# Optimization experiments

Measured on AMD Instinct MI355X. Metric: run time of the kernel, lower is better.

The kernel has to match this reference:

```python
import jax, jax.numpy as jnp
import numpy as np

WIN, DIL, PAD, H = 5, 1, 2, 8  # window, dilation, unfold padding, num_heads
C = 256
EPS = 1e-5

def _ln(z, g, b):
    m = jnp.mean(z, axis=-1, keepdims=True)
    v = jnp.mean((z - m) ** 2, axis=-1, keepdims=True)
    return (z - m) * jax.lax.rsqrt(v + EPS) * g + b

def setup_inputs() -> dict:
    key = jax.random.key(0)
    ks = jax.random.split(key, 16)
    s = 0.02
    d = {
        'x': jax.random.normal(ks[0], (32, C, 64, 25), jnp.float32),
        'ln1_g': jnp.ones((C,), jnp.float32), 'ln1_b': jnp.zeros((C,), jnp.float32),
        'q_w': jax.random.normal(ks[1], (C, C)) * s, 'q_b': jnp.zeros((C,)),
        'qa_w': jax.random.normal(ks[2], (C, H)) * s, 'qa_b': jnp.zeros((H,)),
        'k_w': jax.random.normal(ks[3], (C, C)) * s, 'k_b': jnp.zeros((C,)),
        'ka_w': jax.random.normal(ks[4], (C, H)) * s, 'ka_b': jnp.zeros((H,)),
        'v_w': jax.random.normal(ks[5], (C, C)) * s, 'v_b': jnp.zeros((C,)),
        't_w': jax.random.normal(ks[6], (C, C)) * s, 't_b': jnp.zeros((C,)),
        'p_w': jax.random.normal(ks[7], (C, C)) * s, 'p_b': jnp.zeros((C,)),
        'ffn_g': jnp.ones((C,)), 'ffn_b': jnp.zeros((C,)),
        'w1': jax.random.normal(ks[8], (C, C)) * s, 'b1': jnp.zeros((C,)),
        'w2': jax.random.normal(ks[9], (C, C)) * s, 'b2': jnp.zeros((C,)),
    }
    return d

def reference(x, ln1_g, ln1_b, q_w, q_b, qa_w, qa_b, k_w, k_b, ka_w, ka_b,
              v_w, v_b, t_w, t_b, p_w, p_b, ffn_g, ffn_b, w1, b1, w2, b2):
    N, Cc, T, V = x.shape
    hc = Cc // H
    scale = 1.0 / np.sqrt(hc)
    B, L = N * T, WIN * V
    xp = jnp.pad(x, ((0, 0), (0, 0), (PAD, PAD), (0, 0)))
    win = jnp.stack([xp[:, :, k * DIL:k * DIL + T, :] for k in range(WIN)], axis=2)  # (N,C,W,T,V)
    wx = win.transpose(0, 3, 2, 4, 1).reshape(B, L, Cc)
    nx = _ln(wx, ln1_g, ln1_b)
    # attention: softmax-pooled query
    q = nx @ q_w + q_b                                      # (B,L,C)
    qw = jax.nn.softmax(((q @ qa_w + qa_b) * scale).transpose(0, 2, 1), axis=-1)  # (B,H,L)
    qh = q.reshape(B, L, H, hc).transpose(0, 2, 1, 3)       # (B,H,L,hc)
    pq = jnp.einsum('bhl,bhld->bhd', qw, qh)                # (B,H,hc)
    k_ = nx @ k_w + k_b
    kq = k_ * pq.reshape(B, 1, Cc)
    kw = jax.nn.softmax(((kq @ ka_w + ka_b) * scale).transpose(0, 2, 1), axis=-1)
    kh = k_.reshape(B, L, H, hc).transpose(0, 2, 1, 3)
    pk = jnp.einsum('bhl,bhld->bhd', kw, kh)                # (B,H,hc)
    v_ = nx @ v_w + v_b
    vh = v_.reshape(B, L, H, hc).transpose(0, 2, 1, 3)
    kv = (vh * pk[:, :, None, :]).transpose(0, 2, 1, 3).reshape(B, L, Cc)
    kvh = (kv @ t_w + t_b).reshape(B, L, H, hc).transpose(0, 2, 1, 3)
    att = ((kvh + qh).transpose(0, 2, 1, 3).reshape(B, L, Cc)) @ p_w + p_b
    # average over window, residual with flattened x
    att = att.reshape(B, WIN, V, Cc).mean(axis=1)           # (B,V,C)
    att = att + x.transpose(0, 2, 3, 1).reshape(B, V, Cc)
    # FFN residual block
    f = _ln(att, ffn_g, ffn_b)
    f = jax.nn.gelu(f @ w1 + b1, approximate=False) @ w2 + b2
    y = f + att
    return y.reshape(N, T, V, Cc).transpose(0, 3, 1, 2)     # (N,C,T,V)
```

## Files before the change

### kernel.cpp

```cpp
#include <hip/hip_runtime.h>
#include <hip/hip_bf16.h>

typedef unsigned short u16b;
typedef __attribute__((ext_vector_type(8))) short short8;
typedef __attribute__((ext_vector_type(4))) float floatx4;

#define DEV static __device__ __forceinline__

DEV float sh2f(unsigned short s) { union { unsigned u; float f; } c; c.u = ((unsigned)s) << 16; return c.f; }
DEV unsigned short f2b(float f) {
    unsigned u = __float_as_uint(f);
    u += 0x7FFF + ((u >> 16) & 1);
    return (unsigned short)(u >> 16);
}

constexpr int O_LN1G = 0, O_LN1B = 256, O_QB = 512, O_KB = 768, O_VB = 1024,
              O_TB = 1280, O_PB = 1536, O_FFNG = 1792, O_FFNB = 2048,
              O_B1 = 2304, O_B2 = 2560, O_QAB = 2816, O_KAB = 2824,
              O_QAW = 2832, O_KAW = 4880, O_CV = 6928;

__global__ void detect_k(const unsigned* __restrict__ xw, int* __restrict__ flag) {
    __shared__ int cnt;
    if (threadIdx.x == 0) cnt = 0;
    __syncthreads();
    int my = 0;
    for (int i = threadIdx.x; i < 4096; i += 256) {
        unsigned w = xw[i];
        unsigned e0 = (w >> 7) & 0xFFu;
        if (e0 >= 0xC0u) my++;
    }
    atomicAdd(&cnt, my);
    __syncthreads();
    if (threadIdx.x == 0) flag[0] = (cnt > 64) ? 1 : 0;
}

DEV unsigned short load_cvt(const void* src, size_t idx, int fp32) {
    return fp32 ? f2b(((const float*)src)[idx]) : ((const u16b*)src)[idx];
}

struct VecTab { const void* p[15]; int off[15]; int n[15]; };

__global__ __launch_bounds__(256)
void convert_vecs_k(VecTab tab, const int* __restrict__ flag, u16b* __restrict__ sv) {
    int e = blockIdx.x, fp32 = flag[0];
    const void* s = tab.p[e];
    int n = tab.n[e], off = tab.off[e];
    for (int i = threadIdx.x; i < n; i += 256)
        sv[off + i] = load_cvt(s, i, fp32);
}

struct W8 { const void* p[8]; unsigned dstoff[8]; unsigned rstride[8]; };

__global__ void wtrans_k(W8 tab, u16b* __restrict__ base, const int* __restrict__ flag) {
    __shared__ u16b tile[32][33];
    int fp32 = flag[0];
    const void* src = tab.p[blockIdx.z];
    u16b* dst = base + tab.dstoff[blockIdx.z];
    unsigned rs = tab.rstride[blockIdx.z];
    int c0 = blockIdx.x * 32, r0 = blockIdx.y * 32;
    int tx = threadIdx.x, ty = threadIdx.y;
#pragma unroll
    for (int i = 0; i < 32; i += 8)
        tile[ty + i][tx] = load_cvt(src, (size_t)(r0 + ty + i) * 256 + c0 + tx, fp32);
    __syncthreads();
#pragma unroll
    for (int i = 0; i < 32; i += 8)
        dst[(size_t)(c0 + ty + i) * rs + r0 + tx] = tile[tx][ty + i];
}

__global__ __launch_bounds__(256)
void transpose_in_k(const void* __restrict__ src, u16b* __restrict__ dst,
                    int rows, int cols, const int* __restrict__ flag) {
    __shared__ u16b tile[32][36];
    int fp32 = flag[0];
    int c0 = blockIdx.x * 32, r0 = blockIdx.y * 32;
    size_t zb = (size_t)blockIdx.z * rows * cols;
    int tid = threadIdx.x;
    int r = tid >> 3, c4 = (tid & 7) * 4;
    size_t sidx = zb + (size_t)(r0 + r) * cols + c0 + c4;
    if (fp32) {
        const float4 f4 = *(const float4*)((const float*)src + sidx);
        tile[r][c4]     = f2b(f4.x);
        tile[r][c4 + 1] = f2b(f4.y);
        tile[r][c4 + 2] = f2b(f4.z);
        tile[r][c4 + 3] = f2b(f4.w);
    } else {
        *(ushort4*)&tile[r][c4] = *(const ushort4*)((const u16b*)src + sidx);
    }
    __syncthreads();
    int c = tid >> 3, r4 = (tid & 7) * 4;
    ushort4 o;
    o.x = tile[r4][c]; o.y = tile[r4 + 1][c]; o.z = tile[r4 + 2][c]; o.w = tile[r4 + 3][c];
    *(ushort4*)&dst[zb + (size_t)(c0 + c) * rows + r0 + r4] = o;
}

__global__ __launch_bounds__(256)
void transpose_out_k(const u16b* __restrict__ src, void* __restrict__ dst,
                     int rows, int cols, const int* __restrict__ flag) {
    __shared__ u16b tile[32][36];
    int fp32 = flag[0];
    int c0 = blockIdx.x * 32, r0 = blockIdx.y * 32;
    size_t zb = (size_t)blockIdx.z * rows * cols;
    int tid = threadIdx.x;
    int r = tid >> 3, c4 = (tid & 7) * 4;
    *(ushort4*)&tile[r][c4] = *(const ushort4*)&src[zb + (size_t)(r0 + r) * cols + c0 + c4];
    __syncthreads();
    int c = tid >> 3, r4 = (tid & 7) * 4;
    size_t didx = zb + (size_t)(c0 + c) * rows + r0 + r4;
    if (fp32) {
        float4 f4;
        f4.x = sh2f(tile[r4][c]);     f4.y = sh2f(tile[r4 + 1][c]);
        f4.z = sh2f(tile[r4 + 2][c]); f4.w = sh2f(tile[r4 + 3][c]);
        *(float4*)((float*)dst + didx) = f4;
    } else {
        ushort4 o;
        o.x = tile[r4][c]; o.y = tile[r4 + 1][c]; o.z = tile[r4 + 2][c]; o.w = tile[r4 + 3][c];
        *(ushort4*)((u16b*)dst + didx) = o;
    }
}

__global__ __launch_bounds__(256)
void rowstats_k(const u16b* __restrict__ src, float2* __restrict__ st,
                int valid, int total) {
    int wv = threadIdx.x >> 6, lane = threadIdx.x & 63;
    int r = blockIdx.x * 4 + wv;
    if (r >= total) return;
    if (r >= valid) { if (lane == 0) st[r] = make_float2(0.f, 0.f); return; }
    int c = lane * 4;
    ushort4 raw = *(const ushort4*)&src[(size_t)r * 256 + c];
    float x0 = sh2f(raw.x), x1 = sh2f(raw.y), x2 = sh2f(raw.z), x3 = sh2f(raw.w);
    float s  = x0 + x1 + x2 + x3;
    float sq = x0 * x0 + x1 * x1 + x2 * x2 + x3 * x3;
#pragma unroll
    for (int o = 32; o; o >>= 1) { s += __shfl_xor(s, o); sq += __shfl_xor(sq, o); }
    float mean = s * (1.f / 256.f);
    float var  = sq * (1.f / 256.f) - mean * mean;
    if (lane == 0) st[r] = make_float2(mean, rsqrtf(var + 1e-5f));
}

__global__ __launch_bounds__(256)
void cvec_k(const u16b* __restrict__ pT, u16b* __restrict__ sv) {
    int j = threadIdx.x;
    float acc = sh2f(sv[O_PB + j]);
    const u16b* row = pT + (size_t)j * 256;
    for (int i = 0; i < 256; i += 8) {
        short8 t8 = *(const short8*)&sv[O_TB + i];
        short8 p8 = *(const short8*)&row[i];
#pragma unroll
        for (int u = 0; u < 8; ++u)
            acc += sh2f((unsigned short)t8[u]) * sh2f((unsigned short)p8[u]);
    }
    sv[O_CV + j] = f2b(acc);
}

template <int EPI, int LNA>
__global__ __launch_bounds__(256)
void gemm256(const u16b* __restrict__ A, int aStride, int K,
             const u16b* __restrict__ Wt,
             const u16b* __restrict__ bias, const u16b* __restrict__ addm,
             u16b* __restrict__ out, size_t osParam,
             const float2* __restrict__ stats,
             const u16b* __restrict__ gvec, const u16b* __restrict__ bvec) {
    __shared__ u16b As[128 * 72];
    __shared__ u16b Bs[128 * 72];
    __shared__ float sg[256], sb[256];
    const int tid = threadIdx.x;
    const int m0 = blockIdx.x * 128, n0 = blockIdx.y * 128;
    const int wv = tid >> 6, lane = tid & 63;
    const int wrow = (wv >> 1) * 64, wcol = (wv & 1) * 64;
    const int fr = lane & 15;
    const int fq = lane >> 4;
    floatx4 acc[4][4];
    const floatx4 zero = {0.f, 0.f, 0.f, 0.f};
#pragma unroll
    for (int i = 0; i < 4; ++i)
#pragma unroll
        for (int j = 0; j < 4; ++j) acc[i][j] = zero;

    float2 strow[4];
    if (LNA) {
        sg[tid] = sh2f(gvec[tid]);
        sb[tid] = sh2f(bvec[tid]);
#pragma unroll
        for (int kk = 0; kk < 4; ++kk) strow[kk] = stats[m0 + (tid >> 3) + kk * 32];
        __syncthreads();
    }

    for (int kt = 0; kt < K; kt += 64) {
#pragma unroll
        for (int kk = 0; kk < 4; ++kk) {
            int chunk = tid + kk * 256;
            int row = chunk >> 3, col = (chunk & 7) * 8;
            union { uint4 u; unsigned short h[8]; } rw;
            rw.u = *(const uint4*)&A[(size_t)(m0 + row) * aStride + kt + col];
            if (LNA) {
#pragma unroll
                for (int j = 0; j < 8; ++j) {
                    float f = sh2f(rw.h[j]);
                    f = (f - strow[kk].x) * strow[kk].y * sg[kt + col + j] + sb[kt + col + j];
                    rw.h[j] = f2b(f);
                }
            }
            *(uint4*)&As[row * 72 + col] = rw.u;
            *(uint4*)&Bs[row * 72 + col] = *(const uint4*)&Wt[(size_t)(n0 + row) * K + kt + col];
        }
        __syncthreads();
#pragma unroll
        for (int s = 0; s < 2; ++s) {
            short8 af[4], bfr[4];
#pragma unroll
            for (int i = 0; i < 4; ++i)
                af[i] = *(short8*)&As[(wrow + i * 16 + fr) * 72 + s * 32 + fq * 8];
#pragma unroll
            for (int j = 0; j < 4; ++j)
                bfr[j] = *(short8*)&Bs[(wcol + j * 16 + fr) * 72 + s * 32 + fq * 8];
#pragma unroll
            for (int i = 0; i < 4; ++i)
#pragma unroll
                for (int j = 0; j < 4; ++j)
                    acc[i][j] = __builtin_amdgcn_mfma_f32_16x16x32_bf16(af[i], bfr[j], acc[i][j], 0, 0, 0);
        }
        __syncthreads();
    }
    float bv[4];
#pragma unroll
    for (int j = 0; j < 4; ++j) bv[j] = bias ? sh2f(bias[n0 + wcol + j * 16 + fr]) : 0.f;
#pragma unroll
    for (int i = 0; i < 4; ++i) {
#pragma unroll
        for (int r = 0; r < 4; ++r) {
            int row = m0 + wrow + i * 16 + fq * 4 + r;
            size_t ro = (size_t)row * 256;
#pragma unroll
            for (int j = 0; j < 4; ++j) {
                int col = n0 + wcol + j * 16 + fr;
                float val = acc[i][j][r] + bv[j];
                if (EPI == 2) val += sh2f(addm[ro + col]);
                if (EPI == 3) val = 0.5f * val * (1.0f + erff(val * 0.70710678118654752f));
                if (EPI == 4)      out[(size_t)(col >> 8) * osParam + ro + (col & 255)] = f2b(val);
                else if (EPI == 0) out[(size_t)row * osParam + col] = f2b(val);
                else               out[ro + col] = f2b(val);
            }
        }
    }
}

DEV void logits_stage(const u16b* __restrict__ S, const u16b* __restrict__ sv,
                      int awoff, int aboff, const float* mult,
                      const int* srow, u16b* su, float* slog, int tid) {
    for (int i = tid; i < 2048; i += 512) {
        int c = i >> 3, h = i & 7;
        float w = sh2f(sv[awoff + i]);
        if (mult) w *= mult[c];
        su[h * 260 + c] = f2b(w);
    }
    __syncthreads();
    int wv = tid >> 6, lane = tid & 63;
    int fr = lane & 15, fq = lane >> 4;
    floatx4 acc = {0.f, 0.f, 0.f, 0.f};
    const u16b* Ar = S + (size_t)srow[wv * 16 + fr] * 256;
#pragma unroll
    for (int s = 0; s < 8; ++s) {
        short8 a  = *(const short8*)&Ar[s * 32 + fq * 8];
        short8 bb = *(const short8*)&su[fr * 260 + s * 32 + fq * 8];
        acc = __builtin_amdgcn_mfma_f32_16x16x32_bf16(a, bb, acc, 0, 0, 0);
    }
    float abv = sh2f(sv[aboff + (fr & 7)]);
    if (fr < 8) {
#pragma unroll
        for (int r = 0; r < 4; ++r)
            slog[(wv * 16 + fq * 4 + r) * 9 + fr] = (acc[r] + abv) * 0.17677669529663687f;
    }
    __syncthreads();
    {
        int h = wv;
        float v0 = (lane < 125) ? slog[lane * 9 + h] : -1e30f;
        float v1 = (lane + 64 < 125) ? slog[(lane + 64) * 9 + h] : -1e30f;
        float mx = fmaxf(v0, v1);
#pragma unroll
        for (int o = 32; o; o >>= 1) mx = fmaxf(mx, __shfl_xor(mx, o));
        float e0 = (lane < 125) ? __expf(v0 - mx) : 0.f;
        float e1 = (lane + 64 < 125) ? __expf(v1 - mx) : 0.f;
        float s = e0 + e1;
#pragma unroll
        for (int o = 32; o; o >>= 1) s += __shfl_xor(s, o);
        float inv = 1.f / s;
        if (lane < 125) slog[lane * 9 + h] = e0 * inv;
        if (lane + 64 < 125) slog[(lane + 64) * 9 + h] = e1 * inv;
    }
    __syncthreads();
}

__global__ __launch_bounds__(512)
void pool_fused(const u16b* __restrict__ qf, const u16b* __restrict__ kf,
                const u16b* __restrict__ vf, const u16b* __restrict__ sv,
                u16b* __restrict__ CB) {
    __shared__ int srow[128];
    __shared__ u16b su[16 * 260];
    __shared__ float slog[128 * 9];
    __shared__ float spool[16 * 260];
    __shared__ float spq[256], spk[256];
    int bid = blockIdx.x;
    int b = ((bid & 7) << 8) | (bid >> 3);
    int n = b >> 6, t = b & 63;
    int tid = threadIdx.x;
    if (tid < 128) {
        int l = tid < 125 ? tid : 124;
        int w = l / 25, v = l - w * 25, tt = t + w - 2;
        srow[tid] = ((unsigned)tt < 64u) ? (n * 64 + tt) * 25 + v : 51200;
    }
    __syncthreads();

    logits_stage(qf, sv, O_QAW, O_QAB, nullptr, srow, su, slog, tid);

    {
        int c8 = (tid & 31) * 8, h = c8 >> 5, ls = tid >> 5;
        float p[8] = {0.f, 0.f, 0.f, 0.f, 0.f, 0.f, 0.f, 0.f};
        for (int v = ls; v < 25; v += 16) {
            float s[8] = {0.f, 0.f, 0.f, 0.f, 0.f, 0.f, 0.f, 0.f};
#pragma unroll
            for (int w = 0; w < 5; ++w) {
                int l = w * 25 + v;
                float wt = slog[l * 9 + h];
                short8 d8 = *(const short8*)&qf[(size_t)srow[l] * 256 + c8];
#pragma unroll
                for (int j = 0; j < 8; ++j) {
                    float f = sh2f((unsigned short)d8[j]);
                    s[j] += f;
                    p[j] += wt * f;
                }
            }
            unsigned short o[8];
#pragma unroll
            for (int j = 0; j < 8; ++j) o[j] = f2b(s[j] * 0.2f);
            *(uint4*)&CB[((size_t)b * 25 + v) * 512 + 256 + c8] = *(uint4*)o;
        }
#pragma unroll
        for (int j = 0; j < 8; ++j) spool[ls * 260 + c8 + j] = p[j];
    }
    __syncthreads();
    if (tid < 256) {
        float s = 0.f;
#pragma unroll
        for (int q = 0; q < 16; ++q) s += spool[q * 260 + tid];
        spq[tid] = s;
    }
    __syncthreads();

    logits_stage(kf, sv, O_KAW, O_KAB, spq, srow, su, slog, tid);

    {
        int c8 = (tid & 31) * 8, h2 = c8 >> 5, ls = tid >> 5;
        float a8[8] = {0.f, 0.f, 0.f, 0.f, 0.f, 0.f, 0.f, 0.f};
        for (int l = ls; l < 125; l += 16) {
            float w = slog[l * 9 + h2];
            short8 d8 = *(const short8*)&kf[(size_t)srow[l] * 256 + c8];
#pragma unroll
            for (int j = 0; j < 8; ++j) a8[j] += w * sh2f((unsigned short)d8[j]);
        }
#pragma unroll
        for (int j = 0; j < 8; ++j) spool[ls * 260 + c8 + j] = a8[j];
    }
    __syncthreads();
    if (tid < 256) {
        float s = 0.f;
#pragma unroll
        for (int q = 0; q < 16; ++q) s += spool[q * 260 + tid];
        spk[tid] = s;
    }
    __syncthreads();

    {
        int c8 = (tid & 31) * 8, ls = tid >> 5;
        for (int v = ls; v < 25; v += 16) {
            float s[8] = {0.f, 0.f, 0.f, 0.f, 0.f, 0.f, 0.f, 0.f};
#pragma unroll
            for (int w = 0; w < 5; ++w) {
                short8 d8 = *(const short8*)&vf[(size_t)srow[w * 25 + v] * 256 + c8];
#pragma unroll
                for (int j = 0; j < 8; ++j) s[j] += sh2f((unsigned short)d8[j]);
            }
            unsigned short o[8];
#pragma unroll
            for (int j = 0; j < 8; ++j) o[j] = f2b(s[j] * 0.2f * spk[c8 + j]);
            *(uint4*)&CB[((size_t)b * 25 + v) * 512 + c8] = *(uint4*)o;
        }
    }
}

extern "C" void kernel_launch(void* const* d_in, const int* in_sizes, int n_in,
                              void* d_out, int out_size, void* d_ws, size_t ws_size,
                              hipStream_t stream) {
    (void)in_sizes; (void)n_in; (void)out_size; (void)ws_size;
    const void* x    = d_in[0];
    const void* ln1g = d_in[1];  const void* ln1b = d_in[2];
    const void* q_w  = d_in[3];  const void* q_b  = d_in[4];
    const void* qa_w = d_in[5];  const void* qa_b = d_in[6];
    const void* k_w  = d_in[7];  const void* k_b  = d_in[8];
    const void* ka_w = d_in[9];  const void* ka_b = d_in[10];
    const void* v_w  = d_in[11]; const void* v_b  = d_in[12];
    const void* t_w  = d_in[13]; const void* t_b  = d_in[14];
    const void* p_w  = d_in[15]; const void* p_b  = d_in[16];
    const void* ffng = d_in[17]; const void* ffnb = d_in[18];
    const void* w1   = d_in[19]; const void* b1   = d_in[20];
    const void* w2   = d_in[21]; const void* b2   = d_in[22];

    char* ws = (char*)d_ws;
    size_t off = 0;
    auto alloc = [&](size_t bytes) { void* p = ws + off; off += (bytes + 255) & ~(size_t)255; return p; };
    const size_t RPAD = 51328;
    int*    flag = (int*)alloc(256);
    u16b*   sv   = (u16b*)alloc(8192 * 2);
    u16b*   wT   = (u16b*)alloc((size_t)7 * 65536 * 2);
    u16b*   cW   = (u16b*)alloc((size_t)256 * 512 * 2);
    u16b*   xT   = (u16b*)alloc(RPAD * 256 * 2);
    u16b*   Bq   = (u16b*)alloc(RPAD * 256 * 2);
    u16b*   Bk   = (u16b*)alloc(RPAD * 256 * 2);
    u16b*   Bv   = (u16b*)alloc(RPAD * 256 * 2);
    u16b*   CB   = (u16b*)alloc((size_t)51200 * 512 * 2);
    u16b*   att  = (u16b*)alloc((size_t)51200 * 256 * 2);
    float2* st1  = (float2*)alloc(RPAD * 8);
    float2* st2  = (float2*)alloc((size_t)51200 * 8);

    u16b* pT  = wT + 3 * 65536;
    u16b* tT  = wT + 4 * 65536;
    u16b* w1T = wT + 5 * 65536;
    u16b* w2T = wT + 6 * 65536;

    detect_k<<<1, 256, 0, stream>>>((const unsigned*)x, flag);
    VecTab tab;
    const void* vp[15] = {ln1g, ln1b, q_b, k_b, v_b, t_b, p_b, ffng, ffnb, b1, b2, qa_b, ka_b, qa_w, ka_w};
    const int vo[15] = {O_LN1G, O_LN1B, O_QB, O_KB, O_VB, O_TB, O_PB, O_FFNG, O_FFNB, O_B1, O_B2, O_QAB, O_KAB, O_QAW, O_KAW};
    const int vn[15] = {256, 256, 256, 256, 256, 256, 256, 256, 256, 256, 256, 8, 8, 2048, 2048};
    for (int i = 0; i < 15; ++i) { tab.p[i] = vp[i]; tab.off[i] = vo[i]; tab.n[i] = vn[i]; }
    convert_vecs_k<<<15, 256, 0, stream>>>(tab, flag, sv);

    dim3 tb(32, 8);
    W8 wt;
    const void* wsrc[8] = {q_w, k_w, v_w, p_w, t_w, w1, w2, p_w};
    for (int i = 0; i < 8; ++i) {
        wt.p[i] = wsrc[i];
        wt.dstoff[i] = (i < 7) ? (unsigned)(i * 65536) : (unsigned)((cW + 256) - wT);
        wt.rstride[i] = (i < 7) ? 256u : 512u;
    }
    wtrans_k<<<dim3(8, 8, 8), tb, 0, stream>>>(wt, wT, flag);
    cvec_k<<<1, 256, 0, stream>>>(pT, sv);
    gemm256<0, 0><<<dim3(2, 2), 256, 0, stream>>>(pT, 256, 256, tT, nullptr, nullptr,
                                                  cW, 512, nullptr, nullptr, nullptr);
    transpose_in_k<<<dim3(50, 8, 32), 256, 0, stream>>>(x, xT, 256, 1600, flag);
    rowstats_k<<<12832, 256, 0, stream>>>(xT, st1, 51200, 51328);
    gemm256<4, 1><<<dim3(401, 6), 256, 0, stream>>>(xT, 256, 256, wT, sv + O_QB, nullptr,
                                                    Bq, RPAD * 256, st1, sv + O_LN1G, sv + O_LN1B);
    pool_fused<<<2048, 512, 0, stream>>>(Bq, Bk, Bv, sv, CB);
    gemm256<2, 0><<<dim3(400, 2), 256, 0, stream>>>(CB, 512, 512, cW, sv + O_CV, xT,
                                                    att, 256, nullptr, nullptr, nullptr);
    rowstats_k<<<12800, 256, 0, stream>>>(att, st2, 51200, 51200);
    gemm256<3, 1><<<dim3(400, 2), 256, 0, stream>>>(att, 256, 256, w1T, sv + O_B1, nullptr,
                                                    Bq, 256, st2, sv + O_FFNG, sv + O_FFNB);
    gemm256<2, 0><<<dim3(400, 2), 256, 0, stream>>>(Bq, 256, 256, w2T, sv + O_B2, att,
                                                    att, 256, nullptr, nullptr, nullptr);
    transpose_out_k<<<dim3(8, 50, 32), 256, 0, stream>>>(att, d_out, 1600, 256, flag);
}
```

Measured before the change: 414.2 us.

## Split pooled attention into per-row Q logits, sliding-window sums and scaled GEMM

Computes the per-row query logits once per token row (lq_k) instead of recomputing them per window with MFMA, since each row appears in up to five windows. The window means of q and v are produced by a separate sliding-sum kernel that reuses running sums along T. The pk scaling of v moves into the A-tile load of the following GEMM through a float table. This cuts redundant loads and compute in pool_fused but adds two kernel launches, extra fp32 buffers and per-element scaling work in the GEMM load path.

```diff
diff --git a/kernel.cpp b/kernel.cpp
--- a/kernel.cpp
+++ b/kernel.cpp
@@ -153,14 +153,93 @@
     sv[O_CV + j] = f2b(acc);
 }
 
-template <int EPI, int LNA>
+__global__ __launch_bounds__(256)
+void lq_k(const u16b* __restrict__ qf, const u16b* __restrict__ sv,
+          float* __restrict__ Lq, int total) {
+    __shared__ float w[2048];
+    int tid = threadIdx.x;
+    for (int i = tid; i < 2048; i += 256) w[i] = sh2f(sv[O_QAW + i]);
+    __syncthreads();
+    int wv = tid >> 6, lane = tid & 63;
+    int r = blockIdx.x * 4 + wv;
+    if (r >= total) return;
+    int c = lane * 4;
+    ushort4 raw = *(const ushort4*)&qf[(size_t)r * 256 + c];
+    float acc[8] = {0.f, 0.f, 0.f, 0.f, 0.f, 0.f, 0.f, 0.f};
+    float xv[4] = {sh2f(raw.x), sh2f(raw.y), sh2f(raw.z), sh2f(raw.w)};
+#pragma unroll
+    for (int j = 0; j < 4; ++j)
+#pragma unroll
+        for (int h = 0; h < 8; ++h) acc[h] += xv[j] * w[(c + j) * 8 + h];
+#pragma unroll
+    for (int o = 32; o; o >>= 1)
+#pragma unroll
+        for (int h = 0; h < 8; ++h) acc[h] += __shfl_xor(acc[h], o);
+    float out = 0.f;
+#pragma unroll
+    for (int h = 0; h < 8; ++h) if (lane == h) out = acc[h];
+    if (lane < 8) Lq[(size_t)r * 8 + lane] = out;
+}
+
+__global__ __launch_bounds__(256)
+void slide_k(const u16b* __restrict__ qf, const u16b* __restrict__ vf,
+             u16b* __restrict__ CB) {
+    int gid = blockIdx.x * 256 + threadIdx.x;
+    int c8 = (gid & 31) * 8;
+    int r1 = gid >> 5;
+    int v  = r1 % 25;
+    int r2 = r1 / 25;
+    int n  = r2 >> 2, ch = r2 & 3;
+    int t0 = ch * 16;
+    const size_t trow = 25 * 256;
+    size_t rb  = ((size_t)(n * 64) * 25 + v) * 256 + c8;
+    size_t pad = (size_t)51200 * 256 + c8;
+
+    auto rq = [&](int tt) -> short8 {
+        return *(const short8*)&qf[((unsigned)tt < 64u) ? rb + (size_t)tt * trow : pad];
+    };
+    auto rv = [&](int tt) -> short8 {
+        return *(const short8*)&vf[((unsigned)tt < 64u) ? rb + (size_t)tt * trow : pad];
+    };
+    float sq[8], sv8[8];
+#pragma unroll
+    for (int j = 0; j < 8; ++j) { sq[j] = 0.f; sv8[j] = 0.f; }
+#pragma unroll
+    for (int k = -2; k <= 2; ++k) {
+        short8 a = rq(t0 + k), b = rv(t0 + k);
+#pragma unroll
+        for (int j = 0; j < 8; ++j) {
+            sq[j]  += sh2f((unsigned short)a[j]);
+            sv8[j] += sh2f((unsigned short)b[j]);
+        }
+    }
+    for (int t = t0;;) {
+        size_t ob = ((size_t)(n * 64 + t) * 25 + v) * 512;
+        unsigned short oq[8], ov[8];
+#pragma unroll
+        for (int j = 0; j < 8; ++j) { oq[j] = f2b(sq[j] * 0.2f); ov[j] = f2b(sv8[j] * 0.2f); }
+        *(uint4*)&CB[ob + 256 + c8] = *(uint4*)oq;
+        *(uint4*)&CB[ob + c8]       = *(uint4*)ov;
+        if (++t == t0 + 16) break;
+        short8 qa = rq(t + 2), qo = rq(t - 3);
+        short8 va = rv(t + 2), vo = rv(t - 3);
+#pragma unroll
+        for (int j = 0; j < 8; ++j) {
+            sq[j]  += sh2f((unsigned short)qa[j]) - sh2f((unsigned short)qo[j]);
+            sv8[j] += sh2f((unsigned short)va[j]) - sh2f((unsigned short)vo[j]);
+        }
+    }
+}
+
+template <int EPI, int LNA, int SCL = 0>
 __global__ __launch_bounds__(256)
 void gemm256(const u16b* __restrict__ A, int aStride, int K,
              const u16b* __restrict__ Wt,
              const u16b* __restrict__ bias, const u16b* __restrict__ addm,
              u16b* __restrict__ out, size_t osParam,
              const float2* __restrict__ stats,
-             const u16b* __restrict__ gvec, const u16b* __restrict__ bvec) {
+             const u16b* __restrict__ gvec, const u16b* __restrict__ bvec,
+             const float* __restrict__ pkTab) {
     __shared__ u16b As[128 * 72];
     __shared__ u16b Bs[128 * 72];
     __shared__ float sg[256], sb[256];
@@ -201,6 +280,22 @@
                     rw.h[j] = f2b(f);
                 }
             }
+            if (SCL) {
+                if (kt < 256) {
+                    unsigned b25 = (unsigned)(m0 + row) / 25u;
+                    const float* pkr = pkTab + ((size_t)b25 << 8) + (kt + col);
+                    float4 p0 = *(const float4*)pkr;
+                    float4 p1 = *(const float4*)(pkr + 4);
+                    rw.h[0] = f2b(sh2f(rw.h[0]) * p0.x);
+                    rw.h[1] = f2b(sh2f(rw.h[1]) * p0.y);
+                    rw.h[2] = f2b(sh2f(rw.h[2]) * p0.z);
+                    rw.h[3] = f2b(sh2f(rw.h[3]) * p0.w);
+                    rw.h[4] = f2b(sh2f(rw.h[4]) * p1.x);
+                    rw.h[5] = f2b(sh2f(rw.h[5]) * p1.y);
+                    rw.h[6] = f2b(sh2f(rw.h[6]) * p1.z);
+                    rw.h[7] = f2b(sh2f(rw.h[7]) * p1.w);
+                }
+            }
             *(uint4*)&As[row * 72 + col] = rw.u;
             *(uint4*)&Bs[row * 72 + col] = *(const uint4*)&Wt[(size_t)(n0 + row) * K + kt + col];
         }
@@ -245,13 +340,30 @@
     }
 }
 
-DEV void logits_stage(const u16b* __restrict__ S, const u16b* __restrict__ sv,
-                      int awoff, int aboff, const float* mult,
-                      const int* srow, u16b* su, float* slog, int tid) {
+DEV void softmax125(float* slog, int tid) {
+    int wv = tid >> 6, lane = tid & 63;
+    int h = wv;
+    float v0 = (lane < 125) ? slog[lane * 9 + h] : -1e30f;
+    float v1 = (lane + 64 < 125) ? slog[(lane + 64) * 9 + h] : -1e30f;
+    float mx = fmaxf(v0, v1);
+#pragma unroll
+    for (int o = 32; o; o >>= 1) mx = fmaxf(mx, __shfl_xor(mx, o));
+    float e0 = (lane < 125) ? __expf(v0 - mx) : 0.f;
+    float e1 = (lane + 64 < 125) ? __expf(v1 - mx) : 0.f;
+    float s = e0 + e1;
+#pragma unroll
+    for (int o = 32; o; o >>= 1) s += __shfl_xor(s, o);
+    float inv = 1.f / s;
+    if (lane < 125) slog[lane * 9 + h] = e0 * inv;
+    if (lane + 64 < 125) slog[(lane + 64) * 9 + h] = e1 * inv;
+}
+
+DEV void logits_mfma(const u16b* __restrict__ S, const u16b* __restrict__ sv,
+                     int awoff, int aboff, const float* mult,
+                     const int* srow, u16b* su, float* slog, int tid) {
     for (int i = tid; i < 2048; i += 512) {
         int c = i >> 3, h = i & 7;
-        float w = sh2f(sv[awoff + i]);
-        if (mult) w *= mult[c];
+        float w = sh2f(sv[awoff + i]) * mult[c];
         su[h * 260 + c] = f2b(w);
     }
     __syncthreads();
@@ -272,34 +384,33 @@
             slog[(wv * 16 + fq * 4 + r) * 9 + fr] = (acc[r] + abv) * 0.17677669529663687f;
     }
     __syncthreads();
-    {
-        int h = wv;
-        float v0 = (lane < 125) ? slog[lane * 9 + h] : -1e30f;
-        float v1 = (lane + 64 < 125) ? slog[(lane + 64) * 9 + h] : -1e30f;
-        float mx = fmaxf(v0, v1);
-#pragma unroll
-        for (int o = 32; o; o >>= 1) mx = fmaxf(mx, __shfl_xor(mx, o));
-        float e0 = (lane < 125) ? __expf(v0 - mx) : 0.f;
-        float e1 = (lane + 64 < 125) ? __expf(v1 - mx) : 0.f;
-        float s = e0 + e1;
-#pragma unroll
-        for (int o = 32; o; o >>= 1) s += __shfl_xor(s, o);
-        float inv = 1.f / s;
-        if (lane < 125) slog[lane * 9 + h] = e0 * inv;
-        if (lane + 64 < 125) slog[(lane + 64) * 9 + h] = e1 * inv;
-    }
-    __syncthreads();
+    softmax125(slog, tid);
+    __syncthreads();
+}
+
+DEV void pool_sum(const u16b* __restrict__ S, const int* srow, const float* slog,
+                  float* spool, int tid) {
+    int c8 = (tid & 31) * 8, h = c8 >> 5, ls = tid >> 5;
+    float a8[8] = {0.f, 0.f, 0.f, 0.f, 0.f, 0.f, 0.f, 0.f};
+    for (int l = ls; l < 125; l += 16) {
+        float w = slog[l * 9 + h];
+        short8 d8 = *(const short8*)&S[(size_t)srow[l] * 256 + c8];
+#pragma unroll
+        for (int j = 0; j < 8; ++j) a8[j] += w * sh2f((unsigned short)d8[j]);
+    }
+#pragma unroll
+    for (int j = 0; j < 8; ++j) spool[ls * 260 + c8 + j] = a8[j];
 }
 
 __global__ __launch_bounds__(512)
 void pool_fused(const u16b* __restrict__ qf, const u16b* __restrict__ kf,
-                const u16b* __restrict__ vf, const u16b* __restrict__ sv,
-                u16b* __restrict__ CB) {
+                const float* __restrict__ Lq, const u16b* __restrict__ sv,
+                float* __restrict__ PK) {
     __shared__ int srow[128];
     __shared__ u16b su[16 * 260];
     __shared__ float slog[128 * 9];
     __shared__ float spool[16 * 260];
-    __shared__ float spq[256], spk[256];
+    __shared__ float spq[256];
     int bid = blockIdx.x;
     int b = ((bid & 7) << 8) | (bid >> 3);
     int n = b >> 6, t = b & 63;
@@ -311,33 +422,15 @@
     }
     __syncthreads();
 
-    logits_stage(qf, sv, O_QAW, O_QAB, nullptr, srow, su, slog, tid);
-
-    {
-        int c8 = (tid & 31) * 8, h = c8 >> 5, ls = tid >> 5;
-        float p[8] = {0.f, 0.f, 0.f, 0.f, 0.f, 0.f, 0.f, 0.f};
-        for (int v = ls; v < 25; v += 16) {
-            float s[8] = {0.f, 0.f, 0.f, 0.f, 0.f, 0.f, 0.f, 0.f};
-#pragma unroll
-            for (int w = 0; w < 5; ++w) {
-                int l = w * 25 + v;
-                float wt = slog[l * 9 + h];
-                short8 d8 = *(const short8*)&qf[(size_t)srow[l] * 256 + c8];
-#pragma unroll
-                for (int j = 0; j < 8; ++j) {
-                    float f = sh2f((unsigned short)d8[j]);
-                    s[j] += f;
-                    p[j] += wt * f;
-                }
-            }
-            unsigned short o[8];
-#pragma unroll
-            for (int j = 0; j < 8; ++j) o[j] = f2b(s[j] * 0.2f);
-            *(uint4*)&CB[((size_t)b * 25 + v) * 512 + 256 + c8] = *(uint4*)o;
-        }
-#pragma unroll
-        for (int j = 0; j < 8; ++j) spool[ls * 260 + c8 + j] = p[j];
-    }
+    for (int i = tid; i < 1000; i += 512) {
+        int l = i >> 3, h = i & 7;
+        slog[l * 9 + h] = (Lq[(size_t)srow[l] * 8 + h] + sh2f(sv[O_QAB + h])) * 0.17677669529663687f;
+    }
+    __syncthreads();
+    softmax125(slog, tid);
+    __syncthreads();
+
+    pool_sum(qf, srow, slog, spool, tid);
     __syncthreads();
     if (tid < 256) {
         float s = 0.f;
@@ -347,44 +440,15 @@
     }
     __syncthreads();
 
-    logits_stage(kf, sv, O_KAW, O_KAB, spq, srow, su, slog, tid);
-
-    {
-        int c8 = (tid & 31) * 8, h2 = c8 >> 5, ls = tid >> 5;
-        float a8[8] = {0.f, 0.f, 0.f, 0.f, 0.f, 0.f, 0.f, 0.f};
-        for (int l = ls; l < 125; l += 16) {
-            float w = slog[l * 9 + h2];
-            short8 d8 = *(const short8*)&kf[(size_t)srow[l] * 256 + c8];
-#pragma unroll
-            for (int j = 0; j < 8; ++j) a8[j] += w * sh2f((unsigned short)d8[j]);
-        }
-#pragma unroll
-        for (int j = 0; j < 8; ++j) spool[ls * 260 + c8 + j] = a8[j];
-    }
+    logits_mfma(kf, sv, O_KAW, O_KAB, spq, srow, su, slog, tid);
+
+    pool_sum(kf, srow, slog, spool, tid);
     __syncthreads();
     if (tid < 256) {
         float s = 0.f;
 #pragma unroll
         for (int q = 0; q < 16; ++q) s += spool[q * 260 + tid];
-        spk[tid] = s;
-    }
-    __syncthreads();
-
-    {
-        int c8 = (tid & 31) * 8, ls = tid >> 5;
-        for (int v = ls; v < 25; v += 16) {
-            float s[8] = {0.f, 0.f, 0.f, 0.f, 0.f, 0.f, 0.f, 0.f};
-#pragma unroll
-            for (int w = 0; w < 5; ++w) {
-                short8 d8 = *(const short8*)&vf[(size_t)srow[w * 25 + v] * 256 + c8];
-#pragma unroll
-                for (int j = 0; j < 8; ++j) s[j] += sh2f((unsigned short)d8[j]);
-            }
-            unsigned short o[8];
-#pragma unroll
-            for (int j = 0; j < 8; ++j) o[j] = f2b(s[j] * 0.2f * spk[c8 + j]);
-            *(uint4*)&CB[((size_t)b * 25 + v) * 512 + c8] = *(uint4*)o;
-        }
+        PK[(size_t)b * 256 + tid] = s;
     }
 }
 
@@ -421,6 +485,8 @@
     u16b*   att  = (u16b*)alloc((size_t)51200 * 256 * 2);
     float2* st1  = (float2*)alloc(RPAD * 8);
     float2* st2  = (float2*)alloc((size_t)51200 * 8);
+    float*  Lq   = (float*)alloc(RPAD * 8 * 4);
+    float*  PK   = (float*)alloc((size_t)2048 * 256 * 4);
 
     u16b* pT  = wT + 3 * 65536;
     u16b* tT  = wT + 4 * 65536;
@@ -446,18 +512,20 @@
     wtrans_k<<<dim3(8, 8, 8), tb, 0, stream>>>(wt, wT, flag);
     cvec_k<<<1, 256, 0, stream>>>(pT, sv);
     gemm256<0, 0><<<dim3(2, 2), 256, 0, stream>>>(pT, 256, 256, tT, nullptr, nullptr,
-                                                  cW, 512, nullptr, nullptr, nullptr);
+                                                  cW, 512, nullptr, nullptr, nullptr, nullptr);
     transpose_in_k<<<dim3(50, 8, 32), 256, 0, stream>>>(x, xT, 256, 1600, flag);
     rowstats_k<<<12832, 256, 0, stream>>>(xT, st1, 51200, 51328);
     gemm256<4, 1><<<dim3(401, 6), 256, 0, stream>>>(xT, 256, 256, wT, sv + O_QB, nullptr,
-                                                    Bq, RPAD * 256, st1, sv + O_LN1G, sv + O_LN1B);
-    pool_fused<<<2048, 512, 0, stream>>>(Bq, Bk, Bv, sv, CB);
-    gemm256<2, 0><<<dim3(400, 2), 256, 0, stream>>>(CB, 512, 512, cW, sv + O_CV, xT,
-                                                    att, 256, nullptr, nullptr, nullptr);
+                                                    Bq, RPAD * 256, st1, sv + O_LN1G, sv + O_LN1B, nullptr);
+    lq_k<<<12832, 256, 0, stream>>>(Bq, sv, Lq, 51328);
+    slide_k<<<400, 256, 0, stream>>>(Bq, Bv, CB);
+    pool_fused<<<2048, 512, 0, stream>>>(Bq, Bk, Lq, sv, PK);
+    gemm256<2, 0, 1><<<dim3(400, 2), 256, 0, stream>>>(CB, 512, 512, cW, sv + O_CV, xT,
+                                                       att, 256, nullptr, nullptr, nullptr, PK);
     rowstats_k<<<12800, 256, 0, stream>>>(att, st2, 51200, 51200);
     gemm256<3, 1><<<dim3(400, 2), 256, 0, stream>>>(att, 256, 256, w1T, sv + O_B1, nullptr,
-                                                    Bq, 256, st2, sv + O_FFNG, sv + O_FFNB);
+                                                    Bq, 256, st2, sv + O_FFNG, sv + O_FFNB, nullptr);
     gemm256<2, 0><<<dim3(400, 2), 256, 0, stream>>>(Bq, 256, 256, w2T, sv + O_B2, att,
-                                                    att, 256, nullptr, nullptr, nullptr);
+                                                    att, 256, nullptr, nullptr, nullptr, nullptr);
     transpose_out_k<<<dim3(8, 50, 32), 256, 0, stream>>>(att, d_out, 1600, 256, flag);
 }
```

After: 473.0 us. +14.2%, slower.
